# Optimization experiments

Hardware: AMD Instinct MI355X
Metric: run time of the kernel (lower is better)

Reference implementation:

```python
import jax, jax.numpy as jnp
import numpy as np

SNR_DB = 20.0   # fixed draw from snr_range=(20, 20)
B_COEF = 0.02   # pink-noise IIR coefficient


def setup_inputs() -> dict:
    key = jax.random.key(0)
    k1, k2 = jax.random.split(key)
    L = 16_777_216  # 2**24 audio samples
    audio = jax.random.normal(k1, (L,), dtype=jnp.float32)
    white = jax.random.normal(k2, (L,), dtype=jnp.float32)  # driving white noise for pink branch
    return {"audio": audio, "white": white}


def _pink_noise(white):
    # p[0] = 0; p[i] = B*w[i] + (1-B)*p[i-1]  -> linear recurrence x_i = a_i*x_{i-1} + u_i
    b = jnp.asarray(B_COEF, white.dtype)
    a = jnp.full(white.shape, 1.0 - B_COEF, white.dtype).at[0].set(0.0)
    u = (b * white).at[0].set(0.0)

    def combine(lhs, rhs):
        a1, u1 = lhs
        a2, u2 = rhs
        return a1 * a2, a2 * u1 + u2

    _, pink = jax.lax.associative_scan(combine, (a, u))
    return pink


def reference(audio, white):
    signal_power = jnp.mean(audio ** 2)
    noise_power = signal_power / (10.0 ** (SNR_DB / 10.0))
    noise = _pink_noise(white) * jnp.sqrt(noise_power)
    return audio + noise
```

## Files before the change

### kernel.cpp

```cpp
#include <hip/hip_runtime.h>
#include <math.h>

#define L_TOTAL (1 << 24)

constexpr float A_COEF = 0.98f;
constexpr float B_COEF = 0.02f;

constexpr int T  = 256;
constexpr int S  = 16;
constexpr int TS = T * S;
constexpr int K_OUT = 4;

__global__ __launch_bounds__(256) void sumsq_kernel(const float4* __restrict__ a4,
                                                    double* __restrict__ acc,
                                                    int n4) {
    int idx    = blockIdx.x * blockDim.x + threadIdx.x;
    int stride = gridDim.x * blockDim.x;
    float s = 0.f;
    for (int i = idx; i < n4; i += stride) {
        float4 v = a4[i];
        s += v.x * v.x + v.y * v.y + v.z * v.z + v.w * v.w;
    }
    #pragma unroll
    for (int o = 32; o > 0; o >>= 1) s += __shfl_down(s, o, 64);
    __shared__ float wsum[4];
    int lane = threadIdx.x & 63;
    int wv   = threadIdx.x >> 6;
    if (lane == 0) wsum[wv] = s;
    __syncthreads();
    if (threadIdx.x == 0) {
        float b = wsum[0] + wsum[1] + wsum[2] + wsum[3];
        atomicAdd(acc, (double)b);
    }
}

__global__ __launch_bounds__(256) void pink_add_kernel(const float* __restrict__ audio,
                                                       const float* __restrict__ white,
                                                       const double* __restrict__ acc,
                                                       float* __restrict__ out) {
    const float scale = (float)sqrt((*acc) * (1.0 / ((double)L_TOTAL * 100.0)));

    __shared__ float lds[TS + TS / 16];
    __shared__ float wave_tot[4];

    const int tid  = threadIdx.x;
    const int lane = tid & 63;
    const int wv   = tid >> 6;
    const int block_start = blockIdx.x * (K_OUT * TS);

    const float a2 = A_COEF * A_COEF;
    const float a4 = a2 * a2;
    const float a8 = a4 * a4;
    const float beta = a8 * a8;
    const float b2 = beta * beta, b4 = b2 * b2, b8 = b4 * b4;
    const float b16 = b8 * b8, b32 = b16 * b16, b64 = b32 * b32;
    const float bpow[6] = {beta, b2, b4, b8, b16, b32};

    const float beta_l = exp2f((float)lane * log2f(beta));
    float b64w = 1.f;
    #pragma unroll
    for (int i = 0; i < 3; ++i) if (wv > i) b64w *= b64;
    const float beta_t = beta_l * b64w;
    const float b256 = b64 * b64 * b64 * b64;

    float c_tile = 0.f;

    for (int k = -1; k < K_OUT; ++k) {
        const int base = block_start + k * TS;
        const int g0   = base + tid * S;

        float w[S];
        if (g0 >= 0) {
            const float4* wp = reinterpret_cast<const float4*>(white + g0);
            #pragma unroll
            for (int q = 0; q < S / 4; ++q) {
                float4 v = wp[q];
                w[4 * q + 0] = v.x; w[4 * q + 1] = v.y;
                w[4 * q + 2] = v.z; w[4 * q + 3] = v.w;
            }
        } else {
            #pragma unroll
            for (int j = 0; j < S; ++j) w[j] = 0.f;
        }
        #pragma unroll
        for (int j = 0; j < S; ++j) w[j] = (g0 + j > 0) ? B_COEF * w[j] : 0.f;

        float p = 0.f;
        #pragma unroll
        for (int j = 0; j < S; ++j) p = fmaf(A_COEF, p, w[j]);

        float W = p;
        #pragma unroll
        for (int i = 0; i < 6; ++i) {
            const int o = 1 << i;
            float up = __shfl_up(W, o, 64);
            if (lane >= o) W = fmaf(bpow[i], up, W);
        }
        if (lane == 63) wave_tot[wv] = W;
        __syncthreads();

        const float G0 = wave_tot[0], G1 = wave_tot[1];
        const float G2 = wave_tot[2], G3 = wave_tot[3];
        const float P1 = G0;
        const float P2 = fmaf(P1, b64, G1);
        const float P3 = fmaf(P2, b64, G2);
        const float P  = (wv == 0) ? 0.f : (wv == 1) ? P1 : (wv == 2) ? P2 : P3;
        const float c_next = fmaf(P3, b64, G3) + c_tile * b256;

        const float Wp = __shfl_up(W, 1, 64);
        const float E  = ((lane == 0) ? 0.f : Wp) + P * beta_l;
        const float C  = E + c_tile * beta_t;
        c_tile = c_next;

        if (k >= 0) {
            float p2 = C;
            const int lb = tid * 17;
            #pragma unroll
            for (int j = 0; j < S; ++j) {
                p2 = fmaf(A_COEF, p2, w[j]);
                lds[lb + j] = p2;
            }
            __syncthreads();

            const float4* ap = reinterpret_cast<const float4*>(audio + base);
            float4*       op = reinterpret_cast<float4*>(out + base);
            #pragma unroll
            for (int q = 0; q < 4; ++q) {
                const int i4 = q * T + tid;
                const int i  = i4 * 4;
                const int pi = i + (i >> 4);
                float4 a = ap[i4];
                float4 r;
                r.x = fmaf(lds[pi + 0], scale, a.x);
                r.y = fmaf(lds[pi + 1], scale, a.y);
                r.z = fmaf(lds[pi + 2], scale, a.z);
                r.w = fmaf(lds[pi + 3], scale, a.w);
                op[i4] = r;
            }
        }
        __syncthreads();
    }
}

extern "C" void kernel_launch(void* const* d_in, const int* in_sizes, int n_in,
                              void* d_out, int out_size, void* d_ws, size_t ws_size,
                              hipStream_t stream) {
    const float* audio = (const float*)d_in[0];
    const float* white = (const float*)d_in[1];
    float* out         = (float*)d_out;
    double* acc        = (double*)d_ws;

    hipMemsetAsync(d_ws, 0, sizeof(double), stream);

    const int n4 = L_TOTAL / 4;
    sumsq_kernel<<<2048, 256, 0, stream>>>((const float4*)audio, acc, n4);

    const int blocks = L_TOTAL / (K_OUT * TS);
    pink_add_kernel<<<blocks, 256, 0, stream>>>(audio, white, acc, out);
}
```

Measured before the change: 199.2 us.

## Replace per-block warm-up tile with truncated 512-sample carry-in reduction

After: 179.8 us. -9.7%, faster.

```diff
diff --git a/kernel.cpp b/kernel.cpp
--- a/kernel.cpp
+++ b/kernel.cpp
@@ -6,10 +6,10 @@
 constexpr float A_COEF = 0.98f;
 constexpr float B_COEF = 0.02f;
 
-constexpr int T  = 256;
-constexpr int S  = 16;
-constexpr int TS = T * S;
-constexpr int K_OUT = 4;
+constexpr int T    = 256;
+constexpr int S    = 16;
+constexpr int TS   = T * S;
+constexpr int WARM = 512;
 
 __global__ __launch_bounds__(256) void sumsq_kernel(const float4* __restrict__ a4,
                                                     double* __restrict__ acc,
@@ -42,11 +42,32 @@
 
     __shared__ float lds[TS + TS / 16];
     __shared__ float wave_tot[4];
+    __shared__ float wsum[4];
 
     const int tid  = threadIdx.x;
     const int lane = tid & 63;
     const int wv   = tid >> 6;
-    const int block_start = blockIdx.x * (K_OUT * TS);
+    const int base = blockIdx.x * TS;
+
+    const float4* ap = reinterpret_cast<const float4*>(audio + base);
+    float4 av[4];
+    #pragma unroll
+    for (int q = 0; q < 4; ++q) av[q] = ap[q * T + tid];
+
+    const float4* wp = reinterpret_cast<const float4*>(white + base + tid * S);
+    float w[S];
+    #pragma unroll
+    for (int q = 0; q < S / 4; ++q) {
+        float4 v = wp[q];
+        w[4 * q + 0] = v.x; w[4 * q + 1] = v.y;
+        w[4 * q + 2] = v.z; w[4 * q + 3] = v.w;
+    }
+
+    float2 wu = make_float2(0.f, 0.f);
+    if (blockIdx.x > 0) {
+        const float2* up = reinterpret_cast<const float2*>(white + base - WARM);
+        wu = up[tid];
+    }
 
     const float a2 = A_COEF * A_COEF;
     const float a4 = a2 * a2;
@@ -61,84 +82,66 @@
     #pragma unroll
     for (int i = 0; i < 3; ++i) if (wv > i) b64w *= b64;
     const float beta_t = beta_l * b64w;
-    const float b256 = b64 * b64 * b64 * b64;
 
-    float c_tile = 0.f;
+    #pragma unroll
+    for (int j = 0; j < S; ++j) w[j] *= B_COEF;
+    if (base == 0 && tid == 0) w[0] = 0.f;
 
-    for (int k = -1; k < K_OUT; ++k) {
-        const int base = block_start + k * TS;
-        const int g0   = base + tid * S;
+    float p = 0.f;
+    #pragma unroll
+    for (int j = 0; j < S; ++j) p = fmaf(A_COEF, p, w[j]);
 
-        float w[S];
-        if (g0 >= 0) {
-            const float4* wp = reinterpret_cast<const float4*>(white + g0);
-            #pragma unroll
-            for (int q = 0; q < S / 4; ++q) {
-                float4 v = wp[q];
-                w[4 * q + 0] = v.x; w[4 * q + 1] = v.y;
-                w[4 * q + 2] = v.z; w[4 * q + 3] = v.w;
-            }
-        } else {
-            #pragma unroll
-            for (int j = 0; j < S; ++j) w[j] = 0.f;
-        }
-        #pragma unroll
-        for (int j = 0; j < S; ++j) w[j] = (g0 + j > 0) ? B_COEF * w[j] : 0.f;
+    float W = p;
+    #pragma unroll
+    for (int i = 0; i < 6; ++i) {
+        const int o = 1 << i;
+        float up = __shfl_up(W, o, 64);
+        if (lane >= o) W = fmaf(bpow[i], up, W);
+    }
 
-        float p = 0.f;
-        #pragma unroll
-        for (int j = 0; j < S; ++j) p = fmaf(A_COEF, p, w[j]);
+    float part = fmaf(A_COEF, B_COEF * wu.x, B_COEF * wu.y);
+    part *= exp2f((float)(255 - tid) * log2f(a2));
+    #pragma unroll
+    for (int o = 32; o > 0; o >>= 1) part += __shfl_down(part, o, 64);
 
-        float W = p;
-        #pragma unroll
-        for (int i = 0; i < 6; ++i) {
-            const int o = 1 << i;
-            float up = __shfl_up(W, o, 64);
-            if (lane >= o) W = fmaf(bpow[i], up, W);
-        }
-        if (lane == 63) wave_tot[wv] = W;
-        __syncthreads();
+    if (lane == 63) wave_tot[wv] = W;
+    if (lane == 0)  wsum[wv] = part;
+    __syncthreads();
 
-        const float G0 = wave_tot[0], G1 = wave_tot[1];
-        const float G2 = wave_tot[2], G3 = wave_tot[3];
-        const float P1 = G0;
-        const float P2 = fmaf(P1, b64, G1);
-        const float P3 = fmaf(P2, b64, G2);
-        const float P  = (wv == 0) ? 0.f : (wv == 1) ? P1 : (wv == 2) ? P2 : P3;
-        const float c_next = fmaf(P3, b64, G3) + c_tile * b256;
+    const float G0 = wave_tot[0], G1 = wave_tot[1];
+    const float G2 = wave_tot[2], G3 = wave_tot[3];
+    const float P1 = G0;
+    const float P2 = fmaf(P1, b64, G1);
+    const float P3 = fmaf(P2, b64, G2);
+    const float P  = (wv == 0) ? 0.f : (wv == 1) ? P1 : (wv == 2) ? P2 : P3;
+    const float Cw = wsum[0] + wsum[1] + wsum[2] + wsum[3];
 
-        const float Wp = __shfl_up(W, 1, 64);
-        const float E  = ((lane == 0) ? 0.f : Wp) + P * beta_l;
-        const float C  = E + c_tile * beta_t;
-        c_tile = c_next;
+    const float Wp = __shfl_up(W, 1, 64);
+    const float E  = ((lane == 0) ? 0.f : Wp) + P * beta_l;
+    const float C  = E + Cw * beta_t;
 
-        if (k >= 0) {
-            float p2 = C;
-            const int lb = tid * 17;
-            #pragma unroll
-            for (int j = 0; j < S; ++j) {
-                p2 = fmaf(A_COEF, p2, w[j]);
-                lds[lb + j] = p2;
-            }
-            __syncthreads();
+    float p2 = C;
+    const int lb = tid * 17;
+    #pragma unroll
+    for (int j = 0; j < S; ++j) {
+        p2 = fmaf(A_COEF, p2, w[j]);
+        lds[lb + j] = p2;
+    }
+    __syncthreads();
 
-            const float4* ap = reinterpret_cast<const float4*>(audio + base);
-            float4*       op = reinterpret_cast<float4*>(out + base);
-            #pragma unroll
-            for (int q = 0; q < 4; ++q) {
-                const int i4 = q * T + tid;
-                const int i  = i4 * 4;
-                const int pi = i + (i >> 4);
-                float4 a = ap[i4];
-                float4 r;
-                r.x = fmaf(lds[pi + 0], scale, a.x);
-                r.y = fmaf(lds[pi + 1], scale, a.y);
-                r.z = fmaf(lds[pi + 2], scale, a.z);
-                r.w = fmaf(lds[pi + 3], scale, a.w);
-                op[i4] = r;
-            }
-        }
-        __syncthreads();
+    float4* op = reinterpret_cast<float4*>(out + base);
+    #pragma unroll
+    for (int q = 0; q < 4; ++q) {
+        const int i4 = q * T + tid;
+        const int i  = i4 * 4;
+        const int pi = i + (i >> 4);
+        float4 a = av[q];
+        float4 r;
+        r.x = fmaf(lds[pi + 0], scale, a.x);
+        r.y = fmaf(lds[pi + 1], scale, a.y);
+        r.z = fmaf(lds[pi + 2], scale, a.z);
+        r.w = fmaf(lds[pi + 3], scale, a.w);
+        op[i4] = r;
     }
 }
 
@@ -153,8 +156,8 @@
     hipMemsetAsync(d_ws, 0, sizeof(double), stream);
 
     const int n4 = L_TOTAL / 4;
-    sumsq_kernel<<<2048, 256, 0, stream>>>((const float4*)audio, acc, n4);
+    sumsq_kernel<<<1024, 256, 0, stream>>>((const float4*)audio, acc, n4);
 
-    const int blocks = L_TOTAL / (K_OUT * TS);
+    const int blocks = L_TOTAL / TS;
     pink_add_kernel<<<blocks, 256, 0, stream>>>(audio, white, acc, out);
 }
```
